# Performance work log

Hardware: AMD Instinct MI355X
Metric: run time of the kernel (lower is better)

## Reference

```python
import jax, jax.numpy as jnp
import numpy as np

KW = 31       # avg_pool kernel
PAD = 15      # padding (count_include_pad=True => divide by KW*KW always)


def _box_avg(x):
    # F.avg_pool2d(x, 31, stride=1, padding=15) with count_include_pad=True
    s = jax.lax.reduce_window(
        x, 0.0, jax.lax.add,
        window_dimensions=(1, 1, KW, KW),
        window_strides=(1, 1, 1, 1),
        padding=((0, 0), (0, 0), (PAD, PAD), (PAD, PAD)))
    return s / (KW * KW)


def setup_inputs() -> dict:
    key = jax.random.key(0)
    k1, k2 = jax.random.split(key)
    B, C, H, W = 64, 1, 512, 512
    pred = jax.random.normal(k1, (B, C, H, W), dtype=jnp.float32)
    mask = jax.random.uniform(k2, (B, C, H, W), dtype=jnp.float32)
    return {"pred": pred, "mask": mask}


def reference(pred, mask):
    weit = 1.0 + 5.0 * jnp.abs(_box_avg(mask) - mask)
    # stable BCE-with-logits, elementwise
    bce = jnp.maximum(pred, 0.0) - pred * mask + jnp.log1p(jnp.exp(-jnp.abs(pred)))
    # NOTE: original passes reduce='none' which PyTorch's legacy handling maps to
    # reduction='mean' -> wbce is a global scalar; the weit normalization cancels.
    wbce = bce.mean()  # scalar, broadcast over [B, C]
    p = jax.nn.sigmoid(pred)
    inter = (p * mask * weit).sum(axis=(2, 3))          # [B, C]
    union = ((p + mask) * weit).sum(axis=(2, 3))        # [B, C]
    wiou = 1.0 - (inter + 1.0) / (union - inter + 1.0)  # [B, C]
    return (wbce + wiou).mean()
```

## Files before the change

### kernel.cpp

```cpp
#include <hip/hip_runtime.h>
#include <math.h>

#define BDIM 64
#define HDIM 512
#define WDIM 512
#define KW   31
#define PAD  15
#define INV_KK (1.0f / 961.0f)
#define TH   128
#define BAND 256
#define NPIX ((size_t)BDIM * HDIM * WDIM)

#define NACC 129

__global__ void zero_acc_kernel(double* acc) {
    int i = threadIdx.x;
    if (i < NACC) acc[i] = 0.0;
}

template<int CTRL, int RMASK>
__device__ __forceinline__ float dpp_add(float p) {
    int t = __builtin_amdgcn_update_dpp(0, __builtin_bit_cast(int, p),
                                        CTRL, RMASK, 0xf, true);
    return p + __builtin_bit_cast(float, t);
}

__device__ __forceinline__ float wave_iscan(float p) {
    p = dpp_add<0x111, 0xf>(p);
    p = dpp_add<0x112, 0xf>(p);
    p = dpp_add<0x114, 0xf>(p);
    p = dpp_add<0x118, 0xf>(p);
    p = dpp_add<0x142, 0xa>(p);
    p = dpp_add<0x143, 0xc>(p);
    return p;
}

__device__ __forceinline__ float wave_iscan30(float p) {
    p = dpp_add<0x111, 0xf>(p);
    p = dpp_add<0x112, 0xf>(p);
    p = dpp_add<0x114, 0xf>(p);
    p = dpp_add<0x118, 0xf>(p);
    p = dpp_add<0x142, 0xa>(p);
    return p;
}

__device__ __forceinline__ float wave_shr1(float p) {
    int t = __builtin_amdgcn_update_dpp(0, __builtin_bit_cast(int, p),
                                        0x138 , 0xf, 0xf, true);
    return __builtin_bit_cast(float, t);
}

__global__ __launch_bounds__(256, 2)
void fused_kernel(const float* __restrict__ pred,
                  const float* __restrict__ mask,
                  double* __restrict__ acc) {
    __shared__ float ring[32][BAND];
    __shared__ float red[3][4];

    const int b    = blockIdx.x;
    const int y0   = blockIdx.y * TH;
    const int tid  = threadIdx.x;
    const int lane = tid & 63;
    const int wv   = tid >> 6;
    const int x    = blockIdx.z * BAND + tid;
    const int s    = blockIdx.z * BAND + wv * 64;

    const float* mbase = mask + (size_t)b * HDIM * WDIM;
    const float* pbase = pred + (size_t)b * HDIM * WDIM;

    const int acol = s - 15 + lane;
    const int bcol = s + 49 + lane;
    const bool a_ok = (acol >= 0) && (acol < WDIM);
    const bool b_ok = (lane < 30) && (bcol < WDIM);
    const int hi_lane = (lane + 30) & 63;

    const int tstart = y0 - PAD;
    const int tend   = y0 + TH - 1 + PAD;

    float vs = 0.f;
    float bce_acc = 0.f, inter_acc = 0.f, uni_acc = 0.f;

    auto load_halo = [&](int t, float& A, float& B) {
        A = 0.f; B = 0.f;
        if ((unsigned)t < (unsigned)HDIM) {
            const float* rp = mbase + (size_t)t * WDIM;
            if (a_ok) A = rp[acol];
            if (b_ok) B = rp[bcol];
        }
    };
    auto load_emit = [&](int t, float& M, float& P) {
        M = 0.f; P = 0.f;
        if (t >= y0 + PAD && t <= tend) {
            const size_t off = (size_t)(t - PAD) * WDIM + x;
            M = mbase[off];
            P = pbase[off];
        }
    };

    auto process = [&](int t, float A, float B, float M, float P, float rr) {
        float pa = wave_iscan(A);
        float pb = wave_iscan30(B);
        const float atot = __builtin_bit_cast(float,
            __builtin_amdgcn_readlane(__builtin_bit_cast(int, pa), 63));
        const float v1 = __shfl(pa, hi_lane);
        const float v2 = __shfl(pb, hi_lane);
        const float Phi = (lane <= 33) ? v1 : (atot + v2);
        const float Plo = wave_shr1(pa);
        const float hs  = Phi - Plo;

        vs += hs - rr;
        ring[t & 31][tid] = hs;

        if (t >= y0 + PAD) {
            const float box  = vs * INV_KK;
            const float weit = 1.f + 5.f * fabsf(box - M);
            const float e1   = __expf(-fabsf(P));
            const float den  = __builtin_amdgcn_rcpf(1.f + e1);
            const float sp   = ((P >= 0.f) ? 1.f : e1) * den;
            const float bce  = fmaxf(P, 0.f) - P * M + __logf(1.f + e1);
            bce_acc   += bce;
            inter_acc += sp * M * weit;
            uni_acc   += (sp + M) * weit;
        }
    };

    float cA0,cB0,cM0,cP0, cA1,cB1,cM1,cP1;
    float nA0,nB0,nM0,nP0, nA1,nB1,nM1,nP1;
    load_halo(tstart,     cA0, cB0); load_emit(tstart,     cM0, cP0);
    load_halo(tstart + 1, cA1, cB1); load_emit(tstart + 1, cM1, cP1);
    load_halo(tstart + 2, nA0, nB0); load_emit(tstart + 2, nM0, nP0);
    load_halo(tstart + 3, nA1, nB1); load_emit(tstart + 3, nM1, nP1);
    float rr0 = 0.f, rr1 = 0.f;

    for (int t = tstart; t <= tend; t += 2) {
        float fA0=0.f,fB0=0.f,fM0=0.f,fP0=0.f, fA1=0.f,fB1=0.f,fM1=0.f,fP1=0.f;
        if (t + 4 <= tend) { load_halo(t + 4, fA0, fB0); load_emit(t + 4, fM0, fP0); }
        if (t + 5 <= tend) { load_halo(t + 5, fA1, fB1); load_emit(t + 5, fM1, fP1); }

        float pr0 = 0.f, pr1 = 0.f;
        if (t + 2 - KW >= tstart) pr0 = ring[(t + 2 - KW) & 31][tid];
        if (t + 3 - KW >= tstart) pr1 = ring[(t + 3 - KW) & 31][tid];

        process(t,     cA0, cB0, cM0, cP0, rr0);
        process(t + 1, cA1, cB1, cM1, cP1, rr1);

        cA0=nA0; cB0=nB0; cM0=nM0; cP0=nP0;
        cA1=nA1; cB1=nB1; cM1=nM1; cP1=nP1;
        nA0=fA0; nB0=fB0; nM0=fM0; nP0=fP0;
        nA1=fA1; nB1=fB1; nM1=fM1; nP1=fP1;
        rr0=pr0; rr1=pr1;
    }

#pragma unroll
    for (int off = 32; off > 0; off >>= 1) {
        bce_acc   += __shfl_down(bce_acc, off);
        inter_acc += __shfl_down(inter_acc, off);
        uni_acc   += __shfl_down(uni_acc, off);
    }
    if (lane == 0) {
        red[0][wv] = bce_acc;
        red[1][wv] = inter_acc;
        red[2][wv] = uni_acc;
    }
    __syncthreads();
    if (threadIdx.x == 0) {
        float bs = 0.f, is = 0.f, us = 0.f;
#pragma unroll
        for (int w = 0; w < 4; ++w) { bs += red[0][w]; is += red[1][w]; us += red[2][w]; }
        atomicAdd(&acc[0],      (double)bs);
        atomicAdd(&acc[1 + b],  (double)is);
        atomicAdd(&acc[65 + b], (double)us);
    }
}

__global__ void finalize_kernel(const double* __restrict__ acc, float* __restrict__ out) {
    const int b = threadIdx.x;
    double inter = acc[1 + b];
    double uni   = acc[65 + b];
    double wiou  = 1.0 - (inter + 1.0) / (uni - inter + 1.0);
#pragma unroll
    for (int off = 32; off > 0; off >>= 1) wiou += __shfl_down(wiou, off);
    if (b == 0) {
        double wbce = acc[0] / (double)NPIX;
        out[0] = (float)(wbce + wiou / (double)BDIM);
    }
}

extern "C" void kernel_launch(void* const* d_in, const int* in_sizes, int n_in,
                              void* d_out, int out_size, void* d_ws, size_t ws_size,
                              hipStream_t stream) {
    const float* pred = (const float*)d_in[0];
    const float* mask = (const float*)d_in[1];
    float* out = (float*)d_out;
    double* acc = (double*)d_ws;

    zero_acc_kernel<<<1, 256, 0, stream>>>(acc);

    dim3 grid(BDIM, HDIM / TH, WDIM / BAND);
    fused_kernel<<<grid, 256, 0, stream>>>(pred, mask, acc);

    finalize_kernel<<<1, 64, 0, stream>>>(acc, out);
}
```

Baseline: 179.6 us.

## Halve row tile, split warmup and emit loops, use branchless clamped halo loads

Cuts the rows per block from 128 to 64 and raises the launch bound to 4 blocks per SM, giving more blocks and more resident waves. The row loop is split into a warmup loop that only builds the vertical running sum and a steady-state loop that emits every row, which removes the per-row emit condition. Halo loads now clamp their column index and multiply by a 0/1 scale instead of branching. Halving the tile raises the share of the 30 warmup rows per block that are recomputed redundantly, and the ring-buffer indexing now relies on a pre-zeroed slot for the first subtraction.

Result: slower. 195.0 us (+8.6%).

```diff
diff --git a/kernel.cpp b/kernel.cpp
--- a/kernel.cpp
+++ b/kernel.cpp
@@ -7,7 +7,7 @@
 #define KW   31
 #define PAD  15
 #define INV_KK (1.0f / 961.0f)
-#define TH   128
+#define TH   64
 #define BAND 256
 #define NPIX ((size_t)BDIM * HDIM * WDIM)
 
@@ -50,7 +50,7 @@
     return __builtin_bit_cast(float, t);
 }
 
-__global__ __launch_bounds__(256, 2)
+__global__ __launch_bounds__(256, 4)
 void fused_kernel(const float* __restrict__ pred,
                   const float* __restrict__ mask,
                   double* __restrict__ acc) {
@@ -68,36 +68,38 @@
     const float* mbase = mask + (size_t)b * HDIM * WDIM;
     const float* pbase = pred + (size_t)b * HDIM * WDIM;
 
-    const int acol = s - 15 + lane;
-    const int bcol = s + 49 + lane;
-    const bool a_ok = (acol >= 0) && (acol < WDIM);
-    const bool b_ok = (lane < 30) && (bcol < WDIM);
+    int acol = s - 15 + lane;
+    int bcol = s + 49 + lane;
+    const float ascale = (acol >= 0 && acol < WDIM) ? 1.f : 0.f;
+    const float bscale = (lane < 30 && bcol < WDIM) ? 1.f : 0.f;
+    acol = min(max(acol, 0), WDIM - 1);
+    bcol = min(max(bcol, 0), WDIM - 1);
     const int hi_lane = (lane + 30) & 63;
 
     const int tstart = y0 - PAD;
+    const int tfirst = y0 + PAD;
     const int tend   = y0 + TH - 1 + PAD;
 
     float vs = 0.f;
     float bce_acc = 0.f, inter_acc = 0.f, uni_acc = 0.f;
 
+    ring[(y0 + 16) & 31][tid] = 0.f;
+
     auto load_halo = [&](int t, float& A, float& B) {
-        A = 0.f; B = 0.f;
-        if ((unsigned)t < (unsigned)HDIM) {
+        if ((unsigned)t < (unsigned)HDIM && t <= tend) {
             const float* rp = mbase + (size_t)t * WDIM;
-            if (a_ok) A = rp[acol];
-            if (b_ok) B = rp[bcol];
-        }
+            A = rp[acol] * ascale;
+            B = rp[bcol] * bscale;
+        } else { A = 0.f; B = 0.f; }
     };
     auto load_emit = [&](int t, float& M, float& P) {
-        M = 0.f; P = 0.f;
-        if (t >= y0 + PAD && t <= tend) {
+        if (t <= tend) {
             const size_t off = (size_t)(t - PAD) * WDIM + x;
             M = mbase[off];
             P = pbase[off];
-        }
-    };
-
-    auto process = [&](int t, float A, float B, float M, float P, float rr) {
+        } else { M = 0.f; P = 0.f; }
+    };
+    auto hscan = [&](float A, float B) -> float {
         float pa = wave_iscan(A);
         float pb = wave_iscan30(B);
         const float atot = __builtin_bit_cast(float,
@@ -106,49 +108,81 @@
         const float v2 = __shfl(pb, hi_lane);
         const float Phi = (lane <= 33) ? v1 : (atot + v2);
         const float Plo = wave_shr1(pa);
-        const float hs  = Phi - Plo;
-
-        vs += hs - rr;
-        ring[t & 31][tid] = hs;
-
-        if (t >= y0 + PAD) {
-            const float box  = vs * INV_KK;
-            const float weit = 1.f + 5.f * fabsf(box - M);
-            const float e1   = __expf(-fabsf(P));
-            const float den  = __builtin_amdgcn_rcpf(1.f + e1);
-            const float sp   = ((P >= 0.f) ? 1.f : e1) * den;
-            const float bce  = fmaxf(P, 0.f) - P * M + __logf(1.f + e1);
-            bce_acc   += bce;
-            inter_acc += sp * M * weit;
-            uni_acc   += (sp + M) * weit;
-        }
-    };
-
-    float cA0,cB0,cM0,cP0, cA1,cB1,cM1,cP1;
-    float nA0,nB0,nM0,nP0, nA1,nB1,nM1,nP1;
-    load_halo(tstart,     cA0, cB0); load_emit(tstart,     cM0, cP0);
-    load_halo(tstart + 1, cA1, cB1); load_emit(tstart + 1, cM1, cP1);
-    load_halo(tstart + 2, nA0, nB0); load_emit(tstart + 2, nM0, nP0);
-    load_halo(tstart + 3, nA1, nB1); load_emit(tstart + 3, nM1, nP1);
-    float rr0 = 0.f, rr1 = 0.f;
-
-    for (int t = tstart; t <= tend; t += 2) {
-        float fA0=0.f,fB0=0.f,fM0=0.f,fP0=0.f, fA1=0.f,fB1=0.f,fM1=0.f,fP1=0.f;
-        if (t + 4 <= tend) { load_halo(t + 4, fA0, fB0); load_emit(t + 4, fM0, fP0); }
-        if (t + 5 <= tend) { load_halo(t + 5, fA1, fB1); load_emit(t + 5, fM1, fP1); }
-
-        float pr0 = 0.f, pr1 = 0.f;
-        if (t + 2 - KW >= tstart) pr0 = ring[(t + 2 - KW) & 31][tid];
-        if (t + 3 - KW >= tstart) pr1 = ring[(t + 3 - KW) & 31][tid];
-
-        process(t,     cA0, cB0, cM0, cP0, rr0);
-        process(t + 1, cA1, cB1, cM1, cP1, rr1);
-
-        cA0=nA0; cB0=nB0; cM0=nM0; cP0=nP0;
-        cA1=nA1; cB1=nB1; cM1=nM1; cP1=nP1;
-        nA0=fA0; nB0=fB0; nM0=fM0; nP0=fP0;
-        nA1=fA1; nB1=fB1; nM1=fM1; nP1=fP1;
-        rr0=pr0; rr1=pr1;
+        return Phi - Plo;
+    };
+    auto emit = [&](float M, float P) {
+        const float box  = vs * INV_KK;
+        const float weit = 1.f + 5.f * fabsf(box - M);
+        const float e1   = __expf(-fabsf(P));
+        const float den  = __builtin_amdgcn_rcpf(1.f + e1);
+        const float sp   = ((P >= 0.f) ? 1.f : e1) * den;
+        const float bce  = fmaxf(P, 0.f) - P * M + __logf(1.f + e1);
+        bce_acc   += bce;
+        inter_acc += sp * M * weit;
+        uni_acc   += (sp + M) * weit;
+    };
+
+    float cA0, cB0, cA1, cB1, nA0, nB0, nA1, nB1;
+    load_halo(tstart,     cA0, cB0);
+    load_halo(tstart + 1, cA1, cB1);
+    load_halo(tstart + 2, nA0, nB0);
+    load_halo(tstart + 3, nA1, nB1);
+    float cM0, cP0, cM1, cP1, nM0, nP0, nM1, nP1;
+    load_emit(tfirst,     cM0, cP0);
+    load_emit(tfirst + 1, cM1, cP1);
+    load_emit(tfirst + 2, nM0, nP0);
+    load_emit(tfirst + 3, nM1, nP1);
+
+    for (int t = tstart; t < tfirst; t += 2) {
+        float fA0, fB0, fA1, fB1;
+        load_halo(t + 4, fA0, fB0);
+        load_halo(t + 5, fA1, fB1);
+        {
+            const float h = hscan(cA0, cB0);
+            vs += h;
+            ring[t & 31][tid] = h;
+        }
+        {
+            const float h = hscan(cA1, cB1);
+            vs += h;
+            ring[(t + 1) & 31][tid] = h;
+        }
+        cA0 = nA0; cB0 = nB0; cA1 = nA1; cB1 = nB1;
+        nA0 = fA0; nB0 = fB0; nA1 = fA1; nB1 = fB1;
+    }
+
+    float rr0 = 0.f;
+    float rr1 = ring[(tfirst + 2) & 31][tid];
+
+#pragma unroll 2
+    for (int t = tfirst; t < tend; t += 2) {
+        float fA0, fB0, fA1, fB1, fM0, fP0, fM1, fP1;
+        load_halo(t + 4, fA0, fB0);
+        load_halo(t + 5, fA1, fB1);
+        load_emit(t + 4, fM0, fP0);
+        load_emit(t + 5, fM1, fP1);
+
+        const float pr0 = ring[(t + 3) & 31][tid];
+        const float pr1 = ring[(t + 4) & 31][tid];
+
+        {
+            const float h = hscan(cA0, cB0);
+            vs += h - rr0;
+            ring[t & 31][tid] = h;
+            emit(cM0, cP0);
+        }
+        {
+            const float h = hscan(cA1, cB1);
+            vs += h - rr1;
+            ring[(t + 1) & 31][tid] = h;
+            emit(cM1, cP1);
+        }
+
+        cA0 = nA0; cB0 = nB0; cA1 = nA1; cB1 = nB1;
+        cM0 = nM0; cP0 = nP0; cM1 = nM1; cP1 = nP1;
+        nA0 = fA0; nB0 = fB0; nA1 = fA1; nB1 = fB1;
+        nM0 = fM0; nP0 = fP0; nM1 = fM1; nP1 = fP1;
+        rr0 = pr0; rr1 = pr1;
     }
 
 #pragma unroll
```
